# Kernel tuning notes

Hardware: AMD Instinct MI355X
Metric: run time of the kernel (lower is better)

## Reference

```python
import jax, jax.numpy as jnp
import numpy as np

SIZES = {"a": 1024, "b": 512, "c": 2048}
OUT = 1024
N_STREAMS = 3
EPS = 1e-5


def _layer_norm(x, w, b):
    mu = jnp.mean(x, axis=-1, keepdims=True)
    var = jnp.mean(jnp.square(x - mu), axis=-1, keepdims=True)
    return (x - mu) * jax.lax.rsqrt(var + EPS) * w + b


def setup_inputs() -> dict:
    key = jax.random.key(0)
    ks = iter(jax.random.split(key, 32))
    B = 32768
    inp = {}
    for name, d in SIZES.items():
        inp[f"x_{name}"] = jax.random.normal(next(ks), (B, d), dtype=jnp.float32)
        inp[f"ln_w_{name}"] = jnp.ones((d,), dtype=jnp.float32)
        inp[f"ln_b_{name}"] = jnp.zeros((d,), dtype=jnp.float32)
        inp[f"W_{name}"] = jax.random.normal(next(ks), (d, OUT), dtype=jnp.float32) / np.sqrt(d)
        inp[f"b_{name}"] = jnp.zeros((OUT,), dtype=jnp.float32)
        # gating linear: size -> n_streams * gate_size (gate_size = OUT, pointwise)
        inp[f"Wg_{name}"] = 0.005 * jax.random.normal(next(ks), (d, N_STREAMS * OUT), dtype=jnp.float32)
        inp[f"bg_{name}"] = jnp.zeros((N_STREAMS * OUT,), dtype=jnp.float32)
    return inp


def reference(x_a, ln_w_a, ln_b_a, W_a, b_a, Wg_a, bg_a,
              x_b, ln_w_b, ln_b_b, W_b, b_b, Wg_b, bg_b,
              x_c, ln_w_c, ln_b_c, W_c, b_c, Wg_c, bg_c):
    xs = [x_a, x_b, x_c]
    lns = [(ln_w_a, ln_b_a), (ln_w_b, ln_b_b), (ln_w_c, ln_b_c)]
    lins = [(W_a, b_a), (W_b, b_b), (W_c, b_c)]
    gats = [(Wg_a, bg_a), (Wg_b, bg_b), (Wg_c, bg_c)]

    gate_logits = 0.0
    outputs = []
    for x, (lw, lb), (W, b), (Wg, bg) in zip(xs, lns, lins, gats):
        f = jax.nn.relu(_layer_norm(x, lw, lb))          # [B, d]
        outputs.append(f @ W + b)                         # [B, OUT]
        gate_logits = gate_logits + (f @ Wg + bg)         # [B, 3*OUT]

    B = x_a.shape[0]
    gate = jax.nn.softmax(gate_logits.reshape(B, N_STREAMS, OUT), axis=1)  # [B,3,OUT]
    out = sum(gate[:, i] * outputs[i] for i in range(N_STREAMS))
    return out
```

## Files before the change

### kernel.cpp

```cpp
#include <hip/hip_runtime.h>
#include <hip/hip_bf16.h>
#include <stdint.h>

#define B_ROWS 32768
#define KTOT   3584
#define NC     6144
#define OUT_N  1024

typedef unsigned short ushort_t;
typedef __attribute__((ext_vector_type(8))) short bf16x8;
typedef __attribute__((ext_vector_type(4))) float f32x4;

__device__ __forceinline__ float b2f(unsigned short u) {
    union { unsigned int i; float f; } x; x.i = ((unsigned int)u) << 16; return x.f;
}
__device__ __forceinline__ unsigned short f2b(float f) {
    union { float f; unsigned int i; } x; x.f = f;
    unsigned int r = x.i + 0x7fffu + ((x.i >> 16) & 1u);
    return (unsigned short)(r >> 16);
}

__device__ __forceinline__ void gload_lds16(const void* g, void* l) {
    auto g1 = reinterpret_cast<const __attribute__((address_space(1))) char*>(
        reinterpret_cast<uintptr_t>(g));
    auto l3 = reinterpret_cast<__attribute__((address_space(3))) char*>(
        (uint32_t)reinterpret_cast<uintptr_t>(l));
    __builtin_amdgcn_global_load_lds(g1, l3, 16, 0, 0);
}

template<int OFF>
__device__ __forceinline__ bf16x8 dsr(uint32_t addr) {
    bf16x8 d;
    asm volatile("ds_read_b128 %0, %1 offset:%2" : "=v"(d) : "v"(addr), "i"(OFF));
    return d;
}

__global__ __launch_bounds__(256) void pack_wt_kernel(
    const float* __restrict__ Wa, const float* __restrict__ Wga,
    const float* __restrict__ Wb, const float* __restrict__ Wgb,
    const float* __restrict__ Wc, const float* __restrict__ Wgc,
    ushort_t* __restrict__ WT)
{
    int s = blockIdx.y;
    const float *Ws, *Wgs; int d, koff;
    if (s == 0)      { Ws = Wa; Wgs = Wga; d = 1024; koff = 0;    }
    else if (s == 1) { Ws = Wb; Wgs = Wgb; d = 512;  koff = 1024; }
    else             { Ws = Wc; Wgs = Wgc; d = 2048; koff = 1536; }
    int kt = blockIdx.x >> 6;
    int ntile = blockIdx.x & 63;
    if (kt >= (d >> 6)) return;
    int k0 = kt * 64, n0 = ntile * 64;
    const float* src; int ld, ncol0;
    if (n0 < 1024) { src = Ws;  ld = 1024; ncol0 = n0; }
    else           { src = Wgs; ld = 3072; ncol0 = n0 - 1024; }

    __shared__ float tile[64][65];
    int tx = threadIdx.x & 63, ty = threadIdx.x >> 6;
    for (int r = ty; r < 64; r += 4)
        tile[r][tx] = src[(size_t)(k0 + r) * ld + ncol0 + tx];
    __syncthreads();
    for (int r = ty; r < 64; r += 4)
        WT[(size_t)(n0 + r) * KTOT + koff + k0 + tx] = f2b(tile[tx][r]);
}

__global__ __launch_bounds__(256) void pack_bias_kernel(
    const float* __restrict__ ba, const float* __restrict__ bb, const float* __restrict__ bc,
    const float* __restrict__ bga, const float* __restrict__ bgb, const float* __restrict__ bgc,
    float* __restrict__ bias)
{
    int i = blockIdx.x * 256 + threadIdx.x;
    if (i >= NC) return;
    float v;
    if (i < 1024)      v = ba[i];
    else if (i < 2048) v = bb[i - 1024];
    else if (i < 3072) v = bc[i - 2048];
    else { int g = i - 3072; v = bga[g] + bgb[g] + bgc[g]; }
    bias[i] = v;
}

__global__ __launch_bounds__(256) void ln_relu_kernel(
    const float* __restrict__ xa, const float* __restrict__ xb, const float* __restrict__ xc,
    const float* __restrict__ wa, const float* __restrict__ wb, const float* __restrict__ wc,
    const float* __restrict__ ba, const float* __restrict__ bb, const float* __restrict__ bc,
    ushort_t* __restrict__ F)
{
    int row = blockIdx.x;
    int s = blockIdx.y;
    const float *x, *w, *b; int d, koff;
    if (s == 0)      { x = xa; w = wa; b = ba; d = 1024; koff = 0;    }
    else if (s == 1) { x = xb; w = wb; b = bb; d = 512;  koff = 1024; }
    else             { x = xc; w = wc; b = bc; d = 2048; koff = 1536; }
    const float* xr = x + (size_t)row * d;
    int tid = threadIdx.x;

    float s1 = 0.f, s2 = 0.f;
    for (int i = tid * 4; i < d; i += 1024) {
        float4 v = *(const float4*)(xr + i);
        s1 += v.x + v.y + v.z + v.w;
        s2 += v.x * v.x + v.y * v.y + v.z * v.z + v.w * v.w;
    }
    for (int o = 32; o > 0; o >>= 1) {
        s1 += __shfl_down(s1, o, 64);
        s2 += __shfl_down(s2, o, 64);
    }
    __shared__ float red1[4], red2[4], bcast[2];
    int wv = tid >> 6, ln = tid & 63;
    if (ln == 0) { red1[wv] = s1; red2[wv] = s2; }
    __syncthreads();
    if (tid == 0) {
        float t1 = red1[0] + red1[1] + red1[2] + red1[3];
        float t2 = red2[0] + red2[1] + red2[2] + red2[3];
        float mean = t1 / d;
        float var = t2 / d - mean * mean;
        bcast[0] = mean;
        bcast[1] = rsqrtf(var + 1e-5f);
    }
    __syncthreads();
    float mean = bcast[0], rstd = bcast[1];

    ushort_t* Fr = F + (size_t)row * KTOT + koff;
    for (int i = tid * 4; i < d; i += 1024) {
        float4 v  = *(const float4*)(xr + i);
        float4 wv4 = *(const float4*)(w + i);
        float4 bv4 = *(const float4*)(b + i);
        float o0 = fmaxf(0.f, (v.x - mean) * rstd * wv4.x + bv4.x);
        float o1 = fmaxf(0.f, (v.y - mean) * rstd * wv4.y + bv4.y);
        float o2 = fmaxf(0.f, (v.z - mean) * rstd * wv4.z + bv4.z);
        float o3 = fmaxf(0.f, (v.w - mean) * rstd * wv4.w + bv4.w);
        union { ushort_t u[4]; uint2 v2; } pk;
        pk.u[0] = f2b(o0); pk.u[1] = f2b(o1); pk.u[2] = f2b(o2); pk.u[3] = f2b(o3);
        *(uint2*)(Fr + i) = pk.v2;
    }
}

__global__ __launch_bounds__(512, 2) void gemm_kernel(
    const ushort_t* __restrict__ F, const ushort_t* __restrict__ WT,
    const float* __restrict__ bias, ushort_t* __restrict__ C)
{
    extern __shared__ ushort_t lds_u16[];

    int bid = blockIdx.x;
    int xcd = bid & 7;
    int local = bid >> 3;
    int rp = local / 3;
    int jj = local - rp * 3;
    int j;
    if (xcd < 4) j = (jj == 0) ? xcd : (jj == 1) ? 8 + xcd : 12 + xcd;
    else         j = (jj == 0) ? xcd : (jj == 1) ? 12 + xcd : 16 + xcd;

    int row0 = rp * 256;
    int n0, koff, klen, c0;
    if (j < 4)       { n0 = j * 256;            koff = 0;    klen = 1024; c0 = j * 256; }
    else if (j < 8)  { n0 = (j - 4) * 256;      koff = 1024; klen = 512;  c0 = 1024 + (j - 4) * 256; }
    else if (j < 12) { n0 = (j - 8) * 256;      koff = 1536; klen = 2048; c0 = 2048 + (j - 8) * 256; }
    else             { n0 = 1024 + (j - 12) * 256; koff = 0; klen = 3584; c0 = 3072 + (j - 12) * 256; }

    int tid = threadIdx.x, w = tid >> 6, l = tid & 63;
    int wm0 = (w >> 2) * 128;
    int wn0 = (w & 3) * 64;

    int srow = w * 32 + (l >> 3);
    int scol = (((l & 7) ^ (l >> 3)) << 3);
    const ushort_t* Ag = F  + (size_t)(row0 + srow) * KTOT + koff + scol;
    const ushort_t* Bg = WT + (size_t)(n0   + srow) * KTOT + koff + scol;

    uint32_t lds_base = (uint32_t)(uintptr_t)lds_u16;
    uint32_t ldsStA = lds_base + (uint32_t)w * 4096u;

#define STG_A(SELOFF, kt, JJ0) do {                                              \
        gload_lds16(Ag + (size_t)(kt) * 64 + (size_t)(JJ0) * 8 * KTOT,           \
                    (void*)(uintptr_t)(ldsStA + (SELOFF) + (JJ0) * 1024u));      \
        gload_lds16(Ag + (size_t)(kt) * 64 + (size_t)((JJ0) + 1) * 8 * KTOT,     \
                    (void*)(uintptr_t)(ldsStA + (SELOFF) + ((JJ0) + 1) * 1024u)); } while (0)
#define STG_B(SELOFF, kt, JJ0) do {                                              \
        gload_lds16(Bg + (size_t)(kt) * 64 + (size_t)(JJ0) * 8 * KTOT,           \
                    (void*)(uintptr_t)(ldsStA + 32768u + (SELOFF) + (JJ0) * 1024u)); \
        gload_lds16(Bg + (size_t)(kt) * 64 + (size_t)((JJ0) + 1) * 8 * KTOT,     \
                    (void*)(uintptr_t)(ldsStA + 32768u + (SELOFF) + ((JJ0) + 1) * 1024u)); } while (0)

    int rl = l & 15;
    int c16_0 = ((l >> 4)    ) ^ (l & 7);
    int c16_1 = ((l >> 4) + 4) ^ (l & 7);
    uint32_t aA0 = lds_base + (uint32_t)((wm0 + rl) * 128 + c16_0 * 16);
    uint32_t aA1 = lds_base + (uint32_t)((wm0 + rl) * 128 + c16_1 * 16);
    uint32_t aB0 = lds_base + 32768u + (uint32_t)((wn0 + rl) * 128 + c16_0 * 16);
    uint32_t aB1 = lds_base + 32768u + (uint32_t)((wn0 + rl) * 128 + c16_1 * 16);

#define WAITL(N) do { asm volatile("s_waitcnt lgkmcnt(" #N ")" ::: "memory");   \
                      __builtin_amdgcn_sched_barrier(0); } while (0)

#define MFMA8(AV, BV, MI0, NI0) do {                                            \
        __builtin_amdgcn_s_setprio(1);                                          \
        _Pragma("unroll")                                                       \
        for (int mi = 0; mi < 4; ++mi)                                          \
            _Pragma("unroll")                                                   \
            for (int ni = 0; ni < 2; ++ni)                                      \
                acc[(MI0)+mi][(NI0)+ni] = __builtin_amdgcn_mfma_f32_16x16x32_bf16( \
                    AV[mi], BV[ni], acc[(MI0)+mi][(NI0)+ni], 0, 0, 0);          \
        __builtin_amdgcn_s_setprio(0);                                          \
    } while (0)

    f32x4 acc[8][4];
    #pragma unroll
    for (int mi = 0; mi < 8; ++mi)
        #pragma unroll
        for (int ni = 0; ni < 4; ++ni)
            acc[mi][ni] = (f32x4){0.f, 0.f, 0.f, 0.f};

    int nkt = klen >> 6;

    STG_A(0u, 0, 0); STG_A(0u, 0, 2); STG_B(0u, 0, 0); STG_B(0u, 0, 2);
    asm volatile("s_waitcnt vmcnt(0)" ::: "memory");
    __builtin_amdgcn_s_barrier();

    for (int t = 0; t < nkt; ++t) {
        const uint32_t co  = (t & 1) ? 65536u : 0u;
        const uint32_t no_ = co ^ 65536u;
        uint32_t A0 = aA0 + co, A1 = aA1 + co, B0 = aB0 + co, B1 = aB1 + co;

        if (t + 1 < nkt) {
            STG_A(no_, t + 1, 0); STG_A(no_, t + 1, 2);
            STG_B(no_, t + 1, 0); STG_B(no_, t + 1, 2);
        }

        bf16x8 alo0[4], alo1[4], ahi0[4], ahi1[4];
        bf16x8 blo0[2], blo1[2], bhi0[2], bhi1[2];

        alo0[0] = dsr<0>(A0); alo0[1] = dsr<2048>(A0);
        alo0[2] = dsr<4096>(A0); alo0[3] = dsr<6144>(A0);
        blo0[0] = dsr<0>(B0); blo0[1] = dsr<2048>(B0);
        bhi0[0] = dsr<4096>(B0); bhi0[1] = dsr<6144>(B0);
        alo1[0] = dsr<0>(A1); alo1[1] = dsr<2048>(A1);
        alo1[2] = dsr<4096>(A1); alo1[3] = dsr<6144>(A1);
        blo1[0] = dsr<0>(B1); blo1[1] = dsr<2048>(B1);

        WAITL(8);
        MFMA8(alo0, blo0, 0, 0);
        bhi1[0] = dsr<4096>(B1); bhi1[1] = dsr<6144>(B1);

        WAITL(8);
        MFMA8(alo0, bhi0, 0, 2);
        ahi0[0] = dsr<8192>(A0);  ahi0[1] = dsr<10240>(A0);
        ahi0[2] = dsr<12288>(A0); ahi0[3] = dsr<14336>(A0);

        WAITL(6);
        MFMA8(alo1, blo1, 0, 0);

        WAITL(4);
        MFMA8(alo1, bhi1, 0, 2);
        ahi1[0] = dsr<8192>(A1);  ahi1[1] = dsr<10240>(A1);
        ahi1[2] = dsr<12288>(A1); ahi1[3] = dsr<14336>(A1);

        WAITL(4);
        MFMA8(ahi0, blo0, 4, 0);

        MFMA8(ahi0, bhi0, 4, 2);

        WAITL(0);
        MFMA8(ahi1, blo1, 4, 0);

        MFMA8(ahi1, bhi1, 4, 2);

        asm volatile("s_waitcnt vmcnt(0)" ::: "memory");
        __builtin_amdgcn_s_barrier();
    }

#undef STG_A
#undef STG_B
#undef WAITL
#undef MFMA8

    #pragma unroll
    for (int ni = 0; ni < 4; ++ni) {
        int col = c0 + wn0 + ni * 16 + rl;
        float bv = bias[col];
        #pragma unroll
        for (int mi = 0; mi < 8; ++mi) {
            int rbase = row0 + wm0 + mi * 16 + (l >> 4) * 4;
            #pragma unroll
            for (int r = 0; r < 4; ++r)
                C[(size_t)(rbase + r) * NC + col] = f2b(acc[mi][ni][r] + bv);
        }
    }
}

typedef __attribute__((ext_vector_type(8))) unsigned short u16x8;

__global__ __launch_bounds__(256) void fuse_kernel(
    const ushort_t* __restrict__ C, float* __restrict__ out)
{
    int t = blockIdx.x * 256 + threadIdx.x;
    int b  = t >> 7;
    int j0 = (t & 127) << 3;
    const ushort_t* Cr = C + (size_t)b * NC;
    u16x8 oa = *(const u16x8*)(Cr + j0);
    u16x8 ob = *(const u16x8*)(Cr + 1024 + j0);
    u16x8 oc = *(const u16x8*)(Cr + 2048 + j0);
    u16x8 g0 = *(const u16x8*)(Cr + 3072 + j0);
    u16x8 g1 = *(const u16x8*)(Cr + 4096 + j0);
    u16x8 g2 = *(const u16x8*)(Cr + 5120 + j0);
    float res[8];
    #pragma unroll
    for (int k = 0; k < 8; ++k) {
        float a0 = b2f(g0[k]), a1 = b2f(g1[k]), a2 = b2f(g2[k]);
        float m = fmaxf(a0, fmaxf(a1, a2));
        float e0 = __expf(a0 - m), e1 = __expf(a1 - m), e2 = __expf(a2 - m);
        float inv = 1.f / (e0 + e1 + e2);
        res[k] = (e0 * b2f(oa[k]) + e1 * b2f(ob[k]) + e2 * b2f(oc[k])) * inv;
    }
    float* op = out + (size_t)b * 1024 + j0;
    *(float4*)op       = (float4){res[0], res[1], res[2], res[3]};
    *(float4*)(op + 4) = (float4){res[4], res[5], res[6], res[7]};
}

extern "C" void kernel_launch(void* const* d_in, const int* in_sizes, int n_in,
                              void* d_out, int out_size, void* d_ws, size_t ws_size,
                              hipStream_t stream)
{
    const float* x_a   = (const float*)d_in[0];
    const float* lnw_a = (const float*)d_in[1];
    const float* lnb_a = (const float*)d_in[2];
    const float* W_a   = (const float*)d_in[3];
    const float* b_a   = (const float*)d_in[4];
    const float* Wg_a  = (const float*)d_in[5];
    const float* bg_a  = (const float*)d_in[6];
    const float* x_b   = (const float*)d_in[7];
    const float* lnw_b = (const float*)d_in[8];
    const float* lnb_b = (const float*)d_in[9];
    const float* W_b   = (const float*)d_in[10];
    const float* b_b   = (const float*)d_in[11];
    const float* Wg_b  = (const float*)d_in[12];
    const float* bg_b  = (const float*)d_in[13];
    const float* x_c   = (const float*)d_in[14];
    const float* lnw_c = (const float*)d_in[15];
    const float* lnb_c = (const float*)d_in[16];
    const float* W_c   = (const float*)d_in[17];
    const float* b_c   = (const float*)d_in[18];
    const float* Wg_c  = (const float*)d_in[19];
    const float* bg_c  = (const float*)d_in[20];

    char* ws = (char*)d_ws;
    ushort_t* F    = (ushort_t*)ws;
    ushort_t* WT   = (ushort_t*)(ws + 234881024);
    ushort_t* Cbuf = (ushort_t*)(ws + 234881024 + 29360128);
    float*    bias = (float*)   (ws + 234881024 + 29360128 + 402653184);

    hipLaunchKernelGGL(pack_wt_kernel, dim3(2048, 3), dim3(256), 0, stream,
                       W_a, Wg_a, W_b, Wg_b, W_c, Wg_c, WT);
    hipLaunchKernelGGL(pack_bias_kernel, dim3(24), dim3(256), 0, stream,
                       b_a, b_b, b_c, bg_a, bg_b, bg_c, bias);
    hipLaunchKernelGGL(ln_relu_kernel, dim3(32768, 3), dim3(256), 0, stream,
                       x_a, x_b, x_c, lnw_a, lnw_b, lnw_c, lnb_a, lnb_b, lnb_c, F);
    hipLaunchKernelGGL(gemm_kernel, dim3(3072), dim3(512), 131072, stream,
                       F, WT, bias, Cbuf);
    hipLaunchKernelGGL(fuse_kernel, dim3(16384), dim3(256), 0, stream,
                       Cbuf, (float*)d_out);
}
```

Measured before the change: 1.116 ms.

## Merge per-stream output GEMM tiles into uniform full-K blocks with mid-loop flushes

The GEMM work split changes from 3072 blocks of uneven K length (per-stream output tiles with K of 1024, 512 or 2048, plus full-K gate tiles) to 2048 blocks that all run the full K of 3584. Output-column blocks now walk all three streams in one K loop and write their accumulators to C at the stream boundaries (k=1024 and k=1536), then reset them. The block-to-XCD mapping is simplified to row-major per XCD. The aim is even load per block, exact fill of the CU slots and fewer block prologues. The cost is pipeline stalls during the mid-loop stores in some blocks.

```diff
diff --git a/kernel.cpp b/kernel.cpp
--- a/kernel.cpp
+++ b/kernel.cpp
@@ -142,18 +142,11 @@
     int bid = blockIdx.x;
     int xcd = bid & 7;
     int local = bid >> 3;
-    int rp = local / 3;
-    int jj = local - rp * 3;
-    int j;
-    if (xcd < 4) j = (jj == 0) ? xcd : (jj == 1) ? 8 + xcd : 12 + xcd;
-    else         j = (jj == 0) ? xcd : (jj == 1) ? 12 + xcd : 16 + xcd;
+    int rp = xcd * 16 + (local >> 4);
+    int j  = local & 15;
 
     int row0 = rp * 256;
-    int n0, koff, klen, c0;
-    if (j < 4)       { n0 = j * 256;            koff = 0;    klen = 1024; c0 = j * 256; }
-    else if (j < 8)  { n0 = (j - 4) * 256;      koff = 1024; klen = 512;  c0 = 1024 + (j - 4) * 256; }
-    else if (j < 12) { n0 = (j - 8) * 256;      koff = 1536; klen = 2048; c0 = 2048 + (j - 8) * 256; }
-    else             { n0 = 1024 + (j - 12) * 256; koff = 0; klen = 3584; c0 = 3072 + (j - 12) * 256; }
+    int n0   = j * 256;
 
     int tid = threadIdx.x, w = tid >> 6, l = tid & 63;
     int wm0 = (w >> 2) * 128;
@@ -161,8 +154,8 @@
 
     int srow = w * 32 + (l >> 3);
     int scol = (((l & 7) ^ (l >> 3)) << 3);
-    const ushort_t* Ag = F  + (size_t)(row0 + srow) * KTOT + koff + scol;
-    const ushort_t* Bg = WT + (size_t)(n0   + srow) * KTOT + koff + scol;
+    const ushort_t* Ag = F  + (size_t)(row0 + srow) * KTOT + scol;
+    const ushort_t* Bg = WT + (size_t)(n0   + srow) * KTOT + scol;
 
     uint32_t lds_base = (uint32_t)(uintptr_t)lds_u16;
     uint32_t ldsStA = lds_base + (uint32_t)w * 4096u;
@@ -207,7 +200,28 @@
         for (int ni = 0; ni < 4; ++ni)
             acc[mi][ni] = (f32x4){0.f, 0.f, 0.f, 0.f};
 
-    int nkt = klen >> 6;
+    auto flush_acc = [&](int c0v) {
+        #pragma unroll
+        for (int ni = 0; ni < 4; ++ni) {
+            int col = c0v + wn0 + ni * 16 + rl;
+            float bv = bias[col];
+            #pragma unroll
+            for (int mi = 0; mi < 8; ++mi) {
+                int rbase = row0 + wm0 + mi * 16 + (l >> 4) * 4;
+                #pragma unroll
+                for (int r = 0; r < 4; ++r)
+                    C[(size_t)(rbase + r) * NC + col] = f2b(acc[mi][ni][r] + bv);
+            }
+        }
+        #pragma unroll
+        for (int mi = 0; mi < 8; ++mi)
+            #pragma unroll
+            for (int ni = 0; ni < 4; ++ni)
+                acc[mi][ni] = (f32x4){0.f, 0.f, 0.f, 0.f};
+    };
+
+    const int nkt = KTOT / 64;
+    const bool is_out = (j < 4);
 
     STG_A(0u, 0, 0); STG_A(0u, 0, 2); STG_B(0u, 0, 0); STG_B(0u, 0, 2);
     asm volatile("s_waitcnt vmcnt(0)" ::: "memory");
@@ -261,6 +275,11 @@
 
         MFMA8(ahi1, bhi1, 4, 2);
 
+        if (is_out) {
+            if (t == 15)      flush_acc(j * 256);
+            else if (t == 23) flush_acc(1024 + j * 256);
+        }
+
         asm volatile("s_waitcnt vmcnt(0)" ::: "memory");
         __builtin_amdgcn_s_barrier();
     }
@@ -270,18 +289,7 @@
 #undef WAITL
 #undef MFMA8
 
-    #pragma unroll
-    for (int ni = 0; ni < 4; ++ni) {
-        int col = c0 + wn0 + ni * 16 + rl;
-        float bv = bias[col];
-        #pragma unroll
-        for (int mi = 0; mi < 8; ++mi) {
-            int rbase = row0 + wm0 + mi * 16 + (l >> 4) * 4;
-            #pragma unroll
-            for (int r = 0; r < 4; ++r)
-                C[(size_t)(rbase + r) * NC + col] = f2b(acc[mi][ni][r] + bv);
-        }
-    }
+    flush_acc(2048 + j * 256);
 }
 
 typedef __attribute__((ext_vector_type(8))) unsigned short u16x8;
@@ -351,7 +359,7 @@
                        b_a, b_b, b_c, bg_a, bg_b, bg_c, bias);
     hipLaunchKernelGGL(ln_relu_kernel, dim3(32768, 3), dim3(256), 0, stream,
                        x_a, x_b, x_c, lnw_a, lnw_b, lnw_c, lnb_a, lnb_b, lnb_c, F);
-    hipLaunchKernelGGL(gemm_kernel, dim3(3072), dim3(512), 131072, stream,
+    hipLaunchKernelGGL(gemm_kernel, dim3(2048), dim3(512), 131072, stream,
                        F, WT, bias, Cbuf);
     hipLaunchKernelGGL(fuse_kernel, dim3(16384), dim3(256), 0, stream,
                        Cbuf, (float*)d_out);
```

Measured after the change: 1.754 ms. 1.57x slower.
